# Kernel optimization log

Measured on AMD Instinct MI355X. Metric: run time of the kernel, lower is better.

Reference implementation:

```python
import jax, jax.numpy as jnp
import numpy as np

N = 100000
E = 3200000
EPS = 1e-5


def setup_inputs() -> dict:
    key = jax.random.key(0)
    ks = jax.random.split(key, 12)
    inp = {
        "x": jax.random.normal(ks[0], (N, 512), dtype=jnp.float32),
        "rows": jax.random.randint(ks[1], (E,), 0, N, dtype=jnp.int32),
        "cols": jax.random.randint(ks[2], (E,), 0, N, dtype=jnp.int32),
        "adj_vals": jax.random.uniform(ks[3], (E,), dtype=jnp.float32),
        "w0": jax.random.normal(ks[4], (512, 256), dtype=jnp.float32) * (1.0 / np.sqrt(512)),
        "b0": jnp.zeros((256,), dtype=jnp.float32),
        "w1": jax.random.normal(ks[5], (256, 128), dtype=jnp.float32) * (1.0 / np.sqrt(256)),
        "b1": jnp.zeros((128,), dtype=jnp.float32),
        "dw0": jax.random.normal(ks[6], (128, 256), dtype=jnp.float32) * (1.0 / np.sqrt(128)),
        "db0": jnp.zeros((256,), dtype=jnp.float32),
        "dw1": jax.random.normal(ks[7], (256, 512), dtype=jnp.float32) * (1.0 / np.sqrt(256)),
        "db1": jnp.zeros((512,), dtype=jnp.float32),
    }
    return inp


def _spmm(rows, cols, vals, h):
    # sparse adj (COO) @ dense h : gather neighbor rows, scale, scatter-add
    return jax.ops.segment_sum(vals[:, None] * h[cols], rows, num_segments=N)


def _bn(h):
    # BatchNorm1d(affine=False, track_running_stats=False): batch stats, biased var
    m = h.mean(axis=0)
    v = h.var(axis=0)
    return (h - m) / jnp.sqrt(v + EPS)


def reference(x, rows, cols, adj_vals, w0, b0, w1, b1, dw0, db0, dw1, db1):
    # encoder: 512 -> 256 (relu, bn) -> 128
    h = _spmm(rows, cols, adj_vals, x @ w0) + b0
    h = _bn(jax.nn.relu(h))
    x_out = _spmm(rows, cols, adj_vals, h @ w1) + b1
    # decoder: relu -> 128 -> 256 (relu, bn) -> 512
    r = jax.nn.relu(x_out)
    r = _spmm(rows, cols, adj_vals, r @ dw0) + db0
    r = _bn(jax.nn.relu(r))
    x_rec = _spmm(rows, cols, adj_vals, r @ dw1) + db1
    return (x_out, x_rec)
```

## Files before the change

### kernel.cpp

```cpp
#include <hip/hip_runtime.h>


typedef _Float16 half2v __attribute__((ext_vector_type(2)));
typedef _Float16 half4v __attribute__((ext_vector_type(4)));
typedef _Float16 half8v __attribute__((ext_vector_type(8)));
typedef float f32x4 __attribute__((ext_vector_type(4)));

__global__ void cast_transpose_w(const float* __restrict__ W, _Float16* __restrict__ Wt,
                                 int Kin, int Kout) {
    const int idx = blockIdx.x * blockDim.x + threadIdx.x;
    if (idx >= Kin * Kout) return;
    const int c = idx / Kin;
    const int k = idx - c * Kin;
    Wt[idx] = (_Float16)W[(size_t)k * Kout + c];
}

template <bool A_F32, bool OUT_F16, bool HAS_BIAS>
__global__ __launch_bounds__(256) void gemm_f16(const void* __restrict__ Av,
                                                const _Float16* __restrict__ Wt,
                                                const float* __restrict__ bias,
                                                void* __restrict__ C,
                                                int Nrows, int Kin, int Kout) {
    __shared__ __align__(16) _Float16 As[128][40];
    __shared__ __align__(16) _Float16 Bs[128][40];
    const int tid = threadIdx.x;
    const int r0 = blockIdx.y * 128;
    const int c0 = blockIdx.x * 128;
    const int w = tid >> 6;
    const int lane = tid & 63;
    const int wm = (w >> 1) << 6;
    const int wn = (w & 1) << 6;
    const int lrow = lane & 15;
    const int lk = (lane >> 4) << 3;

    const _Float16* A16 = (const _Float16*)Av;
    const float* A32 = (const float*)Av;

    f32x4 acc[4][4];
#pragma unroll
    for (int i = 0; i < 4; ++i)
#pragma unroll
        for (int j = 0; j < 4; ++j) acc[i][j] = f32x4{0.f, 0.f, 0.f, 0.f};

    for (int k0 = 0; k0 < Kin; k0 += 32) {
#pragma unroll
        for (int q = 0; q < 2; ++q) {
            const int c = tid + (q << 8);
            const int row = c >> 2;
            const int kc = (c & 3) << 3;
            const int gr = r0 + row;
            half8v av;
            if (A_F32) {
                float4 a0 = make_float4(0.f, 0.f, 0.f, 0.f);
                float4 a1 = make_float4(0.f, 0.f, 0.f, 0.f);
                if (gr < Nrows) {
                    a0 = *(const float4*)(A32 + (size_t)gr * Kin + (k0 + kc));
                    a1 = *(const float4*)(A32 + (size_t)gr * Kin + (k0 + kc) + 4);
                }
                av[0] = (_Float16)a0.x; av[1] = (_Float16)a0.y;
                av[2] = (_Float16)a0.z; av[3] = (_Float16)a0.w;
                av[4] = (_Float16)a1.x; av[5] = (_Float16)a1.y;
                av[6] = (_Float16)a1.z; av[7] = (_Float16)a1.w;
            } else {
                av = half8v{0, 0, 0, 0, 0, 0, 0, 0};
                if (gr < Nrows) av = *(const half8v*)(A16 + (size_t)gr * Kin + (k0 + kc));
            }
            *(half8v*)&As[row][kc] = av;
            const half8v wv = *(const half8v*)(Wt + (size_t)(c0 + row) * Kin + (k0 + kc));
            *(half8v*)&Bs[row][kc] = wv;
        }
        __syncthreads();

        half8v af[4], bf[4];
#pragma unroll
        for (int i = 0; i < 4; ++i) af[i] = *(const half8v*)&As[wm + (i << 4) + lrow][lk];
#pragma unroll
        for (int j = 0; j < 4; ++j) bf[j] = *(const half8v*)&Bs[wn + (j << 4) + lrow][lk];
#pragma unroll
        for (int i = 0; i < 4; ++i)
#pragma unroll
            for (int j = 0; j < 4; ++j)
                acc[i][j] = __builtin_amdgcn_mfma_f32_16x16x32_f16(af[i], bf[j], acc[i][j], 0, 0, 0);
        __syncthreads();
    }

    const int crow0 = r0 + wm + ((lane >> 4) << 2);
    const int ccol0 = c0 + wn + lrow;
#pragma unroll
    for (int j = 0; j < 4; ++j) {
        const int col = ccol0 + (j << 4);
        const float bv = HAS_BIAS ? bias[col] : 0.f;
#pragma unroll
        for (int i = 0; i < 4; ++i) {
            const int rbase = crow0 + (i << 4);
#pragma unroll
            for (int qq = 0; qq < 4; ++qq) {
                const int grow = rbase + qq;
                if (grow < Nrows) {
                    const float val = acc[i][j][qq] + bv;
                    if (OUT_F16)
                        ((_Float16*)C)[(size_t)grow * Kout + col] = (_Float16)val;
                    else
                        ((float*)C)[(size_t)grow * Kout + col] = val;
                }
            }
        }
    }
}

template <bool RELU_A>
__global__ __launch_bounds__(256) void gemm_tile(const float* __restrict__ A,
                                                 const float* __restrict__ W,
                                                 const float* __restrict__ bias,
                                                 float* __restrict__ C,
                                                 int Nrows, int M, int K) {
    __shared__ float Asm[16][68];
    __shared__ float Wsm[16][68];
    const int tid = threadIdx.x;
    const int tx = tid & 15;
    const int ty = tid >> 4;
    const int row0 = blockIdx.y * 64;
    const int col0 = blockIdx.x * 64;

    float acc[4][4];
#pragma unroll
    for (int i = 0; i < 4; ++i)
#pragma unroll
        for (int j = 0; j < 4; ++j) acc[i][j] = 0.f;

    const int ar = tid >> 2;
    const int ak = (tid & 3) << 2;
    const int wr = tid >> 4;
    const int wc = (tid & 15) << 2;

    for (int k0 = 0; k0 < M; k0 += 16) {
        float4 av = make_float4(0.f, 0.f, 0.f, 0.f);
        const int grow = row0 + ar;
        if (grow < Nrows) av = *(const float4*)(A + (size_t)grow * M + (k0 + ak));
        if (RELU_A) {
            av.x = fmaxf(av.x, 0.f); av.y = fmaxf(av.y, 0.f);
            av.z = fmaxf(av.z, 0.f); av.w = fmaxf(av.w, 0.f);
        }
        Asm[ak + 0][ar] = av.x; Asm[ak + 1][ar] = av.y;
        Asm[ak + 2][ar] = av.z; Asm[ak + 3][ar] = av.w;
        float4 wv = *(const float4*)(W + (size_t)(k0 + wr) * K + (col0 + wc));
        *(float4*)&Wsm[wr][wc] = wv;
        __syncthreads();
#pragma unroll
        for (int kk = 0; kk < 16; ++kk) {
            const float4 a = *(const float4*)&Asm[kk][ty << 2];
            const float4 b = *(const float4*)&Wsm[kk][tx << 2];
            acc[0][0] += a.x * b.x; acc[0][1] += a.x * b.y; acc[0][2] += a.x * b.z; acc[0][3] += a.x * b.w;
            acc[1][0] += a.y * b.x; acc[1][1] += a.y * b.y; acc[1][2] += a.y * b.z; acc[1][3] += a.y * b.w;
            acc[2][0] += a.z * b.x; acc[2][1] += a.z * b.y; acc[2][2] += a.z * b.z; acc[2][3] += a.z * b.w;
            acc[3][0] += a.w * b.x; acc[3][1] += a.w * b.y; acc[3][2] += a.w * b.z; acc[3][3] += a.w * b.w;
        }
        __syncthreads();
    }

    float4 bv = make_float4(0.f, 0.f, 0.f, 0.f);
    if (bias != nullptr) bv = *(const float4*)(bias + col0 + (tx << 2));
#pragma unroll
    for (int i = 0; i < 4; ++i) {
        const int grow = row0 + (ty << 2) + i;
        if (grow < Nrows) {
            float4 o = make_float4(acc[i][0] + bv.x, acc[i][1] + bv.y,
                                   acc[i][2] + bv.z, acc[i][3] + bv.w);
            *(float4*)(C + (size_t)grow * K + col0 + (tx << 2)) = o;
        }
    }
}

__global__ void zero_ints(int* __restrict__ p, int n) {
    const int i = blockIdx.x * blockDim.x + threadIdx.x;
    if (i < n) p[i] = 0;
}

__global__ void hist_rows(const int* __restrict__ rows, int* __restrict__ cnt, int E) {
    const int e = blockIdx.x * blockDim.x + threadIdx.x;
    if (e < E) atomicAdd(&cnt[rows[e]], 1);
}

__global__ __launch_bounds__(256) void scan_reduce(const int* __restrict__ cnt,
                                                   int* __restrict__ blockSums, int Nrows) {
    __shared__ int sh[256];
    const int t = threadIdx.x;
    const int idx0 = blockIdx.x * 1024 + t * 4;
    int s = 0;
#pragma unroll
    for (int k = 0; k < 4; ++k) s += (idx0 + k < Nrows) ? cnt[idx0 + k] : 0;
    sh[t] = s;
    __syncthreads();
    for (int d = 128; d > 0; d >>= 1) {
        if (t < d) sh[t] += sh[t + d];
        __syncthreads();
    }
    if (t == 0) blockSums[blockIdx.x] = sh[0];
}

__global__ __launch_bounds__(256) void scan_blocksums(int* __restrict__ blockSums, int NB,
                                                      int* __restrict__ row_start, int Nrows,
                                                      int E) {
    __shared__ int sh[256];
    const int t = threadIdx.x;
    const int v = (t < NB) ? blockSums[t] : 0;
    sh[t] = v;
    __syncthreads();
    for (int d = 1; d < 256; d <<= 1) {
        int add = (t >= d) ? sh[t - d] : 0;
        __syncthreads();
        sh[t] += add;
        __syncthreads();
    }
    if (t < NB) blockSums[t] = sh[t] - v;
    if (t == 0) row_start[Nrows] = E;
}

__global__ __launch_bounds__(256) void scan_final(const int* __restrict__ cnt,
                                                  const int* __restrict__ blockSums,
                                                  int* __restrict__ row_start,
                                                  int* __restrict__ cursor, int Nrows) {
    __shared__ int sh[256];
    const int t = threadIdx.x;
    const int idx0 = blockIdx.x * 1024 + t * 4;
    int c[4];
    int mySum = 0;
#pragma unroll
    for (int k = 0; k < 4; ++k) {
        c[k] = (idx0 + k < Nrows) ? cnt[idx0 + k] : 0;
        mySum += c[k];
    }
    sh[t] = mySum;
    __syncthreads();
    for (int d = 1; d < 256; d <<= 1) {
        int add = (t >= d) ? sh[t - d] : 0;
        __syncthreads();
        sh[t] += add;
        __syncthreads();
    }
    int running = blockSums[blockIdx.x] + sh[t] - mySum;
#pragma unroll
    for (int k = 0; k < 4; ++k) {
        if (idx0 + k < Nrows) {
            row_start[idx0 + k] = running;
            cursor[idx0 + k] = running;
        }
        running += c[k];
    }
}

__global__ void scatter_edges(const int* __restrict__ rows, const int* __restrict__ cols,
                              const float* __restrict__ vals, int* __restrict__ cursor,
                              int2* __restrict__ svc, int E) {
    const int e = blockIdx.x * blockDim.x + threadIdx.x;
    if (e >= E) return;
    const int pos = atomicAdd(&cursor[rows[e]], 1);
    svc[pos] = make_int2(cols[e], __float_as_int(vals[e]));
}

template <int VW, bool RELU_H, bool HAS_BIAS, bool IN_H, bool OUT_H, bool MIRROR>
__global__ __launch_bounds__(256) void spmm_csr(const int* __restrict__ row_start,
                                                const int2* __restrict__ svc,
                                                const void* __restrict__ Hv,
                                                const float* __restrict__ bias,
                                                void* __restrict__ outv,
                                                _Float16* __restrict__ mir,
                                                int Nrows, int F) {
    const int lane = threadIdx.x & 63;
    const int r = blockIdx.x * 4 + (threadIdx.x >> 6);
    if (r >= Nrows) return;
    const int s = row_start[r];
    const int e_end = row_start[r + 1];

    float acc[VW];
#pragma unroll
    for (int i = 0; i < VW; ++i) acc[i] = HAS_BIAS ? bias[lane * VW + i] : 0.f;

    const float* Hf = (const float*)Hv;
    const _Float16* Hh = (const _Float16*)Hv;

    for (int base = s; base < e_end; base += 64) {
        const int n = min(64, e_end - base);
        int cL = 0;
        float vL = 0.f;
        if (lane < n) {
            const int2 p = svc[base + lane];
            cL = p.x;
            vL = __int_as_float(p.y);
        }
        for (int j = 0; j < n; ++j) {
            const int cj = __shfl(cL, j);
            const float vj = __shfl(vL, j);
            float h[VW];
            if (IN_H) {
                const _Float16* hp = Hh + (size_t)cj * F + lane * VW;
                if (VW == 2) {
                    const half2v hv = *(const half2v*)hp;
                    h[0] = (float)hv.x; h[1] = (float)hv.y;
                } else {
#pragma unroll
                    for (int q = 0; q < VW; q += 4) {
                        const half4v hv = *(const half4v*)(hp + q);
                        h[q + 0] = (float)hv.x; h[q + 1] = (float)hv.y;
                        h[q + 2] = (float)hv.z; h[q + 3] = (float)hv.w;
                    }
                }
            } else {
                const float* hp = Hf + (size_t)cj * F + lane * VW;
                if (VW == 2) {
                    const float2 hv = *(const float2*)hp;
                    h[0] = hv.x; h[1] = hv.y;
                } else {
#pragma unroll
                    for (int q = 0; q < VW; q += 4) {
                        const float4 hv = *(const float4*)(hp + q);
                        h[q + 0] = hv.x; h[q + 1] = hv.y; h[q + 2] = hv.z; h[q + 3] = hv.w;
                    }
                }
            }
#pragma unroll
            for (int q = 0; q < VW; ++q) {
                float hq = h[q];
                if (RELU_H) hq = fmaxf(hq, 0.f);
                acc[q] += vj * hq;
            }
        }
    }

    if (OUT_H) {
        _Float16* op = (_Float16*)outv + (size_t)r * F + lane * VW;
        if (VW == 2) {
            half2v o; o.x = (_Float16)acc[0]; o.y = (_Float16)acc[1];
            *(half2v*)op = o;
        } else {
#pragma unroll
            for (int q = 0; q < VW; q += 4) {
                half4v o;
                o.x = (_Float16)acc[q + 0]; o.y = (_Float16)acc[q + 1];
                o.z = (_Float16)acc[q + 2]; o.w = (_Float16)acc[q + 3];
                *(half4v*)(op + q) = o;
            }
        }
    } else {
        float* op = (float*)outv + (size_t)r * F + lane * VW;
        if (VW == 2) {
            *(float2*)op = make_float2(acc[0], acc[1]);
        } else {
#pragma unroll
            for (int q = 0; q < VW; q += 4)
                *(float4*)(op + q) = make_float4(acc[q], acc[q + 1], acc[q + 2], acc[q + 3]);
        }
    }
    if (MIRROR) {
        _Float16* mp = mir + (size_t)r * F + lane * VW;
        if (VW == 2) {
            half2v m;
            m.x = (_Float16)fmaxf(acc[0], 0.f);
            m.y = (_Float16)fmaxf(acc[1], 0.f);
            *(half2v*)mp = m;
        } else {
#pragma unroll
            for (int q = 0; q < VW; q += 4) {
                half4v m;
                m.x = (_Float16)fmaxf(acc[q + 0], 0.f);
                m.y = (_Float16)fmaxf(acc[q + 1], 0.f);
                m.z = (_Float16)fmaxf(acc[q + 2], 0.f);
                m.w = (_Float16)fmaxf(acc[q + 3], 0.f);
                *(half4v*)(mp + q) = m;
            }
        }
    }
}

__global__ void fill_bias(float* __restrict__ out, const float* __restrict__ bias,
                          size_t n4, unsigned maskF4) {
    const size_t i = (size_t)blockIdx.x * blockDim.x + threadIdx.x;
    if (i >= n4) return;
    const int cb = (int)(i & maskF4) << 2;
    ((float4*)out)[i] = *(const float4*)(bias + cb);
}

__global__ void zero_floats4(float* __restrict__ out, size_t n4) {
    const size_t i = (size_t)blockIdx.x * blockDim.x + threadIdx.x;
    if (i >= n4) return;
    ((float4*)out)[i] = make_float4(0.f, 0.f, 0.f, 0.f);
}

template <bool RELU_H>
__global__ void spmm_edges(const int* __restrict__ rows, const int* __restrict__ cols,
                           const float* __restrict__ vals, const float* __restrict__ H,
                           float* __restrict__ out, int E, int F, int log2chunks) {
    const size_t idx = (size_t)blockIdx.x * blockDim.x + threadIdx.x;
    const int e = (int)(idx >> log2chunks);
    if (e >= E) return;
    const int c = (int)(idx & ((1u << log2chunks) - 1u));
    const int dst = rows[e];
    const int src = cols[e];
    const float v = vals[e];
    float4 h = *(const float4*)(H + (size_t)src * F + (c << 2));
    if (RELU_H) {
        h.x = fmaxf(h.x, 0.f); h.y = fmaxf(h.y, 0.f);
        h.z = fmaxf(h.z, 0.f); h.w = fmaxf(h.w, 0.f);
    }
    float* o = out + (size_t)dst * F + (c << 2);
    atomicAdd(o + 0, v * h.x);
    atomicAdd(o + 1, v * h.y);
    atomicAdd(o + 2, v * h.z);
    atomicAdd(o + 3, v * h.w);
}

__global__ void zero_stats(float* __restrict__ p) { p[threadIdx.x] = 0.f; }

__global__ __launch_bounds__(256) void bn_stats(const float* __restrict__ H,
                                                float* __restrict__ stats, int Nrows) {
    __shared__ float shs[4][64][4];
    __shared__ float shq[4][64][4];
    const int t = threadIdx.x;
    const int cg = t & 63;
    const int rs = t >> 6;
    float4 s = make_float4(0.f, 0.f, 0.f, 0.f);
    float4 q = make_float4(0.f, 0.f, 0.f, 0.f);
    for (int n = blockIdx.x * 4 + rs; n < Nrows; n += gridDim.x * 4) {
        float4 h = *(const float4*)(H + (size_t)n * 256 + (cg << 2));
        h.x = fmaxf(h.x, 0.f); h.y = fmaxf(h.y, 0.f);
        h.z = fmaxf(h.z, 0.f); h.w = fmaxf(h.w, 0.f);
        s.x += h.x; s.y += h.y; s.z += h.z; s.w += h.w;
        q.x += h.x * h.x; q.y += h.y * h.y; q.z += h.z * h.z; q.w += h.w * h.w;
    }
    *(float4*)shs[rs][cg] = s;
    *(float4*)shq[rs][cg] = q;
    __syncthreads();
    if (rs == 0) {
        float4 S = make_float4(0.f, 0.f, 0.f, 0.f);
        float4 Q = make_float4(0.f, 0.f, 0.f, 0.f);
#pragma unroll
        for (int k = 0; k < 4; ++k) {
            const float4 a = *(const float4*)shs[k][cg];
            const float4 b = *(const float4*)shq[k][cg];
            S.x += a.x; S.y += a.y; S.z += a.z; S.w += a.w;
            Q.x += b.x; Q.y += b.y; Q.z += b.z; Q.w += b.w;
        }
        const int c0 = cg << 2;
        atomicAdd(&stats[c0 + 0], S.x); atomicAdd(&stats[c0 + 1], S.y);
        atomicAdd(&stats[c0 + 2], S.z); atomicAdd(&stats[c0 + 3], S.w);
        atomicAdd(&stats[256 + c0 + 0], Q.x); atomicAdd(&stats[256 + c0 + 1], Q.y);
        atomicAdd(&stats[256 + c0 + 2], Q.z); atomicAdd(&stats[256 + c0 + 3], Q.w);
    }
}

__global__ void bn_finalize(float* __restrict__ stats, float invN) {
    const int c = threadIdx.x;
    const float m = stats[c] * invN;
    const float q = stats[256 + c] * invN;
    const float var = q - m * m;
    stats[512 + c] = m;
    stats[768 + c] = rsqrtf(var + 1e-5f);
}

template <bool OUT_H>
__global__ void bn_apply(const float* __restrict__ H, const float* __restrict__ stats,
                         void* __restrict__ outv, size_t n4) {
    const size_t i = (size_t)blockIdx.x * blockDim.x + threadIdx.x;
    if (i >= n4) return;
    const int cb = (int)(i & 63u) << 2;
    const float4 h = ((const float4*)H)[i];
    const float4 m = *(const float4*)(stats + 512 + cb);
    const float4 s = *(const float4*)(stats + 768 + cb);
    float4 o;
    o.x = (fmaxf(h.x, 0.f) - m.x) * s.x;
    o.y = (fmaxf(h.y, 0.f) - m.y) * s.y;
    o.z = (fmaxf(h.z, 0.f) - m.z) * s.z;
    o.w = (fmaxf(h.w, 0.f) - m.w) * s.w;
    if (OUT_H) {
        half4v oh;
        oh.x = (_Float16)o.x; oh.y = (_Float16)o.y;
        oh.z = (_Float16)o.z; oh.w = (_Float16)o.w;
        ((half4v*)outv)[i] = oh;
    } else {
        ((float4*)outv)[i] = o;
    }
}

extern "C" void kernel_launch(void* const* d_in, const int* in_sizes, int n_in,
                              void* d_out, int out_size, void* d_ws, size_t ws_size,
                              hipStream_t stream) {
    const float* x    = (const float*)d_in[0];
    const int*   rows = (const int*)d_in[1];
    const int*   cols = (const int*)d_in[2];
    const float* vals = (const float*)d_in[3];
    const float* w0   = (const float*)d_in[4];
    const float* b0   = (const float*)d_in[5];
    const float* w1   = (const float*)d_in[6];
    const float* b1   = (const float*)d_in[7];
    const float* dw0  = (const float*)d_in[8];
    const float* db0  = (const float*)d_in[9];
    const float* dw1  = (const float*)d_in[10];
    const float* db1  = (const float*)d_in[11];

    const int N = in_sizes[0] / 512;
    const int E = in_sizes[1];

    float* xout  = (float*)d_out;
    float* rec   = xout + (size_t)N * 128;
    float* recA  = rec;
    float* recB  = rec + (size_t)N * 256;
    float* wsbig = (float*)d_ws;
    float* stats = wsbig + (size_t)N * 512;

    int*   row_start = (int*)(stats + 1024);
    int*   cursor    = row_start + (N + 1);
    int*   blockSums = cursor + N;
    int2*  svc = (int2*)(((uintptr_t)(blockSums + 256) + 15u) & ~(uintptr_t)15u);

    _Float16* arena = (_Float16*)wsbig;
    _Float16* t0h  = arena + (size_t)N * 512;
    _Float16* t2h  = arena;
    _Float16* t3h  = arena + (size_t)N * 256;
    _Float16* xoh  = arena;
    _Float16* sh   = arena + (size_t)N * 384;
    _Float16* r3h  = arena;
    _Float16* uh   = arena + (size_t)N * 256;
    _Float16* w0t  = arena + (size_t)N * 768;
    _Float16* w1t  = w0t + 512 * 256;
    _Float16* dw0t = w1t + 256 * 128;
    _Float16* dw1t = dw0t + 128 * 256;

    const size_t needed =
        ((size_t)N * 512 + 1024 + (size_t)(N + 1) + (size_t)N + 256) * 4 + 16 +
        (size_t)E * 8;
    const bool use_csr = ws_size >= needed;

    const dim3 blk(256);
    const int NB = (N + 1023) / 1024;
    const int egrid = (E + 255) / 256;
    const int rowgrid = (N + 3) / 4;
    const int gyM = (N + 127) / 128;

    if (use_csr) {
        zero_ints<<<dim3((N + 255) / 256), blk, 0, stream>>>(cursor, N);
        hist_rows<<<dim3(egrid), blk, 0, stream>>>(rows, cursor, E);
        scan_reduce<<<dim3(NB), blk, 0, stream>>>(cursor, blockSums, N);
        scan_blocksums<<<dim3(1), blk, 0, stream>>>(blockSums, NB, row_start, N, E);
        scan_final<<<dim3(NB), blk, 0, stream>>>(cursor, blockSums, row_start, cursor, N);
        scatter_edges<<<dim3(egrid), blk, 0, stream>>>(rows, cols, vals, cursor, svc, E);

        cast_transpose_w<<<dim3((512 * 256 + 255) / 256), blk, 0, stream>>>(w0, w0t, 512, 256);
        cast_transpose_w<<<dim3((256 * 128 + 255) / 256), blk, 0, stream>>>(w1, w1t, 256, 128);
        cast_transpose_w<<<dim3((128 * 256 + 255) / 256), blk, 0, stream>>>(dw0, dw0t, 128, 256);
        cast_transpose_w<<<dim3((256 * 512 + 255) / 256), blk, 0, stream>>>(dw1, dw1t, 256, 512);

        gemm_f16<true, true, false><<<dim3(2, gyM), blk, 0, stream>>>(
            x, w0t, nullptr, t0h, N, 512, 256);
        spmm_csr<4, false, true, true, false, false><<<dim3(rowgrid), blk, 0, stream>>>(
            row_start, svc, t0h, b0, recA, nullptr, N, 256);
        zero_stats<<<dim3(1), dim3(512), 0, stream>>>(stats);
        bn_stats<<<dim3(512), blk, 0, stream>>>(recA, stats, N);
        bn_finalize<<<dim3(1), blk, 0, stream>>>(stats, 1.0f / (float)N);
        bn_apply<true><<<dim3((unsigned)(((size_t)N * 64 + 255) / 256)), blk, 0, stream>>>(
            recA, stats, t2h, (size_t)N * 64);
        gemm_f16<false, true, false><<<dim3(1, gyM), blk, 0, stream>>>(
            t2h, w1t, nullptr, t3h, N, 256, 128);
        spmm_csr<2, false, true, true, false, true><<<dim3(rowgrid), blk, 0, stream>>>(
            row_start, svc, t3h, b1, xout, xoh, N, 128);
        spmm_csr<2, false, false, true, true, false><<<dim3(rowgrid), blk, 0, stream>>>(
            row_start, svc, xoh, nullptr, sh, nullptr, N, 128);
        gemm_f16<false, false, true><<<dim3(2, gyM), blk, 0, stream>>>(
            sh, dw0t, db0, recB, N, 128, 256);
        zero_stats<<<dim3(1), dim3(512), 0, stream>>>(stats);
        bn_stats<<<dim3(512), blk, 0, stream>>>(recB, stats, N);
        bn_finalize<<<dim3(1), blk, 0, stream>>>(stats, 1.0f / (float)N);
        bn_apply<true><<<dim3((unsigned)(((size_t)N * 64 + 255) / 256)), blk, 0, stream>>>(
            recB, stats, r3h, (size_t)N * 64);
        spmm_csr<4, false, false, true, true, false><<<dim3(rowgrid), blk, 0, stream>>>(
            row_start, svc, r3h, nullptr, uh, nullptr, N, 256);
        gemm_f16<false, false, true><<<dim3(4, gyM), blk, 0, stream>>>(
            uh, dw1t, db1, rec, N, 256, 512);
        return;
    }

    const int gy = (N + 63) / 64;
    gemm_tile<false><<<dim3(256 / 64, gy), blk, 0, stream>>>(x, w0, nullptr, recA, N, 512, 256);
    {
        const size_t n4 = (size_t)N * 256 / 4;
        fill_bias<<<dim3((unsigned)((n4 + 255) / 256)), blk, 0, stream>>>(recB, b0, n4, 63u);
        const size_t tot = (size_t)E * 64;
        spmm_edges<false><<<dim3((unsigned)((tot + 255) / 256)), blk, 0, stream>>>(
            rows, cols, vals, recA, recB, E, 256, 6);
    }
    zero_stats<<<dim3(1), dim3(512), 0, stream>>>(stats);
    bn_stats<<<dim3(512), blk, 0, stream>>>(recB, stats, N);
    bn_finalize<<<dim3(1), blk, 0, stream>>>(stats, 1.0f / (float)N);
    bn_apply<false><<<dim3((unsigned)(((size_t)N * 64 + 255) / 256)), blk, 0, stream>>>(
        recB, stats, recA, (size_t)N * 64);
    gemm_tile<false><<<dim3(128 / 64, gy), blk, 0, stream>>>(recA, w1, nullptr, wsbig, N, 256, 128);
    {
        const size_t n4 = (size_t)N * 128 / 4;
        fill_bias<<<dim3((unsigned)((n4 + 255) / 256)), blk, 0, stream>>>(xout, b1, n4, 31u);
        const size_t tot = (size_t)E * 32;
        spmm_edges<false><<<dim3((unsigned)((tot + 255) / 256)), blk, 0, stream>>>(
            rows, cols, vals, wsbig, xout, E, 128, 5);
    }
    {
        const size_t n4 = (size_t)N * 128 / 4;
        zero_floats4<<<dim3((unsigned)((n4 + 255) / 256)), blk, 0, stream>>>(wsbig, n4);
        const size_t tot = (size_t)E * 32;
        spmm_edges<true><<<dim3((unsigned)((tot + 255) / 256)), blk, 0, stream>>>(
            rows, cols, vals, xout, wsbig, E, 128, 5);
    }
    gemm_tile<false><<<dim3(256 / 64, gy), blk, 0, stream>>>(wsbig, dw0, db0, recA, N, 128, 256);
    zero_stats<<<dim3(1), dim3(512), 0, stream>>>(stats);
    bn_stats<<<dim3(512), blk, 0, stream>>>(recA, stats, N);
    bn_finalize<<<dim3(1), blk, 0, stream>>>(stats, 1.0f / (float)N);
    bn_apply<false><<<dim3((unsigned)(((size_t)N * 64 + 255) / 256)), blk, 0, stream>>>(
        recA, stats, recB, (size_t)N * 64);
    {
        const size_t n4 = (size_t)N * 256 / 4;
        zero_floats4<<<dim3((unsigned)((n4 + 255) / 256)), blk, 0, stream>>>(wsbig, n4);
        const size_t tot = (size_t)E * 64;
        spmm_edges<false><<<dim3((unsigned)((tot + 255) / 256)), blk, 0, stream>>>(
            rows, cols, vals, recB, wsbig, E, 256, 6);
    }
    gemm_tile<false><<<dim3(512 / 64, gy), blk, 0, stream>>>(wsbig, dw1, db1, rec, N, 256, 512);
}
```

Baseline: 2.006 ms.

## Two-pass bucketed CSR edge scatter and unroll SpMM gather loop by four

CSR construction now scatters edges in two passes. Edges first go into coarse 128-row buckets, with the local row packed into the high bits of the column index in a temporary buffer. A per-bucket kernel then scatters them into final CSR positions with localized atomics and writes, aiming to cut the random-write and atomic-contention cost of one global scatter. The SpMM inner loop also processes four neighbors per iteration, so more row gathers are in flight at once, at the cost of more registers and a changed summation order. The binned path requires N ≤ 2^17 and reuses the workspace arena as a temporary buffer.

```diff
diff --git a/kernel.cpp b/kernel.cpp
--- a/kernel.cpp
+++ b/kernel.cpp
@@ -249,6 +249,39 @@
     }
 }
 
+__global__ void init_bcur(const int* __restrict__ row_start, int* __restrict__ bcur,
+                          int NBK) {
+    const int b = blockIdx.x * blockDim.x + threadIdx.x;
+    if (b < NBK) bcur[b] = row_start[b << 7];
+}
+
+__global__ void scatter_bucket(const int* __restrict__ rows, const int* __restrict__ cols,
+                               const float* __restrict__ vals, int* __restrict__ bcur,
+                               int2* __restrict__ tmp, int E) {
+    const int e = blockIdx.x * blockDim.x + threadIdx.x;
+    if (e >= E) return;
+    const int r = rows[e];
+    const int pos = atomicAdd(&bcur[r >> 7], 1);
+    tmp[pos] = make_int2(((r & 127) << 17) | cols[e], __float_as_int(vals[e]));
+}
+
+__global__ __launch_bounds__(256) void bucket_scatter(const int2* __restrict__ tmp,
+                                                      const int* __restrict__ row_start,
+                                                      int* __restrict__ cursor,
+                                                      int2* __restrict__ svc, int Nrows) {
+    const int b = blockIdx.x;
+    const int r0 = b << 7;
+    const int rend = min(r0 + 128, Nrows);
+    const int start = row_start[r0];
+    const int end = row_start[rend];
+    for (int i = start + (int)threadIdx.x; i < end; i += 256) {
+        const int2 p = tmp[i];
+        const int row = r0 + ((unsigned)p.x >> 17);
+        const int pos = atomicAdd(&cursor[row], 1);
+        svc[pos] = make_int2(p.x & 0x1FFFF, p.y);
+    }
+}
+
 __global__ void scatter_edges(const int* __restrict__ rows, const int* __restrict__ cols,
                               const float* __restrict__ vals, int* __restrict__ cursor,
                               int2* __restrict__ svc, int E) {
@@ -256,6 +289,37 @@
     if (e >= E) return;
     const int pos = atomicAdd(&cursor[rows[e]], 1);
     svc[pos] = make_int2(cols[e], __float_as_int(vals[e]));
+}
+
+template <int VW, bool IN_H>
+__device__ __forceinline__ void load_hrow(const void* __restrict__ Hv, int cj, int F,
+                                          int lane, float* __restrict__ h) {
+    if (IN_H) {
+        const _Float16* hp = (const _Float16*)Hv + (size_t)cj * F + lane * VW;
+        if (VW == 2) {
+            const half2v hv = *(const half2v*)hp;
+            h[0] = (float)hv.x; h[1] = (float)hv.y;
+        } else {
+#pragma unroll
+            for (int q = 0; q < VW; q += 4) {
+                const half4v hv = *(const half4v*)(hp + q);
+                h[q + 0] = (float)hv.x; h[q + 1] = (float)hv.y;
+                h[q + 2] = (float)hv.z; h[q + 3] = (float)hv.w;
+            }
+        }
+    } else {
+        const float* hp = (const float*)Hv + (size_t)cj * F + lane * VW;
+        if (VW == 2) {
+            const float2 hv = *(const float2*)hp;
+            h[0] = hv.x; h[1] = hv.y;
+        } else {
+#pragma unroll
+            for (int q = 0; q < VW; q += 4) {
+                const float4 hv = *(const float4*)(hp + q);
+                h[q + 0] = hv.x; h[q + 1] = hv.y; h[q + 2] = hv.z; h[q + 3] = hv.w;
+            }
+        }
+    }
 }
 
 template <int VW, bool RELU_H, bool HAS_BIAS, bool IN_H, bool OUT_H, bool MIRROR>
@@ -276,9 +340,6 @@
 #pragma unroll
     for (int i = 0; i < VW; ++i) acc[i] = HAS_BIAS ? bias[lane * VW + i] : 0.f;
 
-    const float* Hf = (const float*)Hv;
-    const _Float16* Hh = (const _Float16*)Hv;
-
     for (int base = s; base < e_end; base += 64) {
         const int n = min(64, e_end - base);
         int cL = 0;
@@ -288,36 +349,39 @@
             cL = p.x;
             vL = __int_as_float(p.y);
         }
-        for (int j = 0; j < n; ++j) {
+        int j = 0;
+        for (; j + 4 <= n; j += 4) {
+            const int c0 = __shfl(cL, j + 0);
+            const int c1 = __shfl(cL, j + 1);
+            const int c2 = __shfl(cL, j + 2);
+            const int c3 = __shfl(cL, j + 3);
+            const float v0 = __shfl(vL, j + 0);
+            const float v1 = __shfl(vL, j + 1);
+            const float v2 = __shfl(vL, j + 2);
+            const float v3 = __shfl(vL, j + 3);
+            float h0[VW], h1[VW], h2[VW], h3[VW];
+            load_hrow<VW, IN_H>(Hv, c0, F, lane, h0);
+            load_hrow<VW, IN_H>(Hv, c1, F, lane, h1);
+            load_hrow<VW, IN_H>(Hv, c2, F, lane, h2);
+            load_hrow<VW, IN_H>(Hv, c3, F, lane, h3);
+#pragma unroll
+            for (int q = 0; q < VW; ++q) {
+                float a0 = h0[q], a1 = h1[q], a2 = h2[q], a3 = h3[q];
+                if (RELU_H) {
+                    a0 = fmaxf(a0, 0.f); a1 = fmaxf(a1, 0.f);
+                    a2 = fmaxf(a2, 0.f); a3 = fmaxf(a3, 0.f);
+                }
+                acc[q] += v0 * a0;
+                acc[q] += v1 * a1;
+                acc[q] += v2 * a2;
+                acc[q] += v3 * a3;
+            }
+        }
+        for (; j < n; ++j) {
             const int cj = __shfl(cL, j);
             const float vj = __shfl(vL, j);
             float h[VW];
-            if (IN_H) {
-                const _Float16* hp = Hh + (size_t)cj * F + lane * VW;
-                if (VW == 2) {
-                    const half2v hv = *(const half2v*)hp;
-                    h[0] = (float)hv.x; h[1] = (float)hv.y;
-                } else {
-#pragma unroll
-                    for (int q = 0; q < VW; q += 4) {
-                        const half4v hv = *(const half4v*)(hp + q);
-                        h[q + 0] = (float)hv.x; h[q + 1] = (float)hv.y;
-                        h[q + 2] = (float)hv.z; h[q + 3] = (float)hv.w;
-                    }
-                }
-            } else {
-                const float* hp = Hf + (size_t)cj * F + lane * VW;
-                if (VW == 2) {
-                    const float2 hv = *(const float2*)hp;
-                    h[0] = hv.x; h[1] = hv.y;
-                } else {
-#pragma unroll
-                    for (int q = 0; q < VW; q += 4) {
-                        const float4 hv = *(const float4*)(hp + q);
-                        h[q + 0] = hv.x; h[q + 1] = hv.y; h[q + 2] = hv.z; h[q + 3] = hv.w;
-                    }
-                }
-            }
+            load_hrow<VW, IN_H>(Hv, cj, F, lane, h);
 #pragma unroll
             for (int q = 0; q < VW; ++q) {
                 float hq = h[q];
@@ -507,12 +571,16 @@
     float* wsbig = (float*)d_ws;
     float* stats = wsbig + (size_t)N * 512;
 
+    const int NBK = (N + 127) / 128;
+
     int*   row_start = (int*)(stats + 1024);
     int*   cursor    = row_start + (N + 1);
     int*   blockSums = cursor + N;
-    int2*  svc = (int2*)(((uintptr_t)(blockSums + 256) + 15u) & ~(uintptr_t)15u);
+    int*   bcur      = blockSums + 256;
+    int2*  svc = (int2*)(((uintptr_t)(bcur + NBK) + 15u) & ~(uintptr_t)15u);
 
     _Float16* arena = (_Float16*)wsbig;
+    int2*     tmpe  = (int2*)wsbig;
     _Float16* t0h  = arena + (size_t)N * 512;
     _Float16* t2h  = arena;
     _Float16* t3h  = arena + (size_t)N * 256;
@@ -526,9 +594,10 @@
     _Float16* dw1t = dw0t + 128 * 256;
 
     const size_t needed =
-        ((size_t)N * 512 + 1024 + (size_t)(N + 1) + (size_t)N + 256) * 4 + 16 +
-        (size_t)E * 8;
+        ((size_t)N * 512 + 1024 + (size_t)(N + 1) + (size_t)N + 256 + (size_t)NBK) * 4 +
+        16 + (size_t)E * 8;
     const bool use_csr = ws_size >= needed;
+    const bool binned = (N <= (1 << 17)) && ((size_t)E * 8 <= (size_t)N * 2048);
 
     const dim3 blk(256);
     const int NB = (N + 1023) / 1024;
@@ -542,7 +611,13 @@
         scan_reduce<<<dim3(NB), blk, 0, stream>>>(cursor, blockSums, N);
         scan_blocksums<<<dim3(1), blk, 0, stream>>>(blockSums, NB, row_start, N, E);
         scan_final<<<dim3(NB), blk, 0, stream>>>(cursor, blockSums, row_start, cursor, N);
-        scatter_edges<<<dim3(egrid), blk, 0, stream>>>(rows, cols, vals, cursor, svc, E);
+        if (binned) {
+            init_bcur<<<dim3((NBK + 255) / 256), blk, 0, stream>>>(row_start, bcur, NBK);
+            scatter_bucket<<<dim3(egrid), blk, 0, stream>>>(rows, cols, vals, bcur, tmpe, E);
+            bucket_scatter<<<dim3(NBK), blk, 0, stream>>>(tmpe, row_start, cursor, svc, N);
+        } else {
+            scatter_edges<<<dim3(egrid), blk, 0, stream>>>(rows, cols, vals, cursor, svc, E);
+        }
 
         cast_transpose_w<<<dim3((512 * 256 + 255) / 256), blk, 0, stream>>>(w0, w0t, 512, 256);
         cast_transpose_w<<<dim3((256 * 128 + 255) / 256), blk, 0, stream>>>(w1, w1t, 256, 128);
```

Result: slower. 2.440 ms (+21.6%).
